# Optimization experiments

Measured on AMD Instinct MI355X. Metric: run time of the kernel, lower is better.

Reference implementation:

```python
import jax, jax.numpy as jnp
import numpy as np

B, D_IN, D_EXP, D_TOW, N_EXP, N_TASK = 16384, 1024, 1024, 512, 8, 4


def setup_inputs() -> dict:
    key = jax.random.key(0)
    ks = jax.random.split(key, 8)
    s_in = 1.0 / np.sqrt(D_IN)
    s_exp = 1.0 / np.sqrt(D_EXP)
    s_tow = 1.0 / np.sqrt(D_TOW)
    return {
        "x": jax.random.normal(ks[0], (B, D_IN), jnp.float32),
        # gate: ParameterList of num_experts vectors of size input_size -> [D_IN, N_EXP] matrix
        "gate_w": jax.random.normal(ks[1], (D_IN, N_EXP), jnp.float32) * s_in,
        # per-expert SLP: Linear(input_size, expert_size) + ReLU
        "exp_w": jax.random.normal(ks[2], (N_EXP, D_IN, D_EXP), jnp.float32) * s_in,
        "exp_b": jax.random.normal(ks[3], (N_EXP, D_EXP), jnp.float32) * 0.01,
        # per-task tower MLP: Linear(expert_size, tower_size) + ReLU + Linear(tower_size, 1)
        "tw1": jax.random.normal(ks[4], (N_TASK, D_EXP, D_TOW), jnp.float32) * s_exp,
        "tb1": jax.random.normal(ks[5], (N_TASK, D_TOW), jnp.float32) * 0.01,
        "tw2": jax.random.normal(ks[6], (N_TASK, D_TOW, 1), jnp.float32) * s_tow,
        "tb2": jax.random.normal(ks[7], (N_TASK, 1), jnp.float32) * 0.01,
    }


def reference(x, gate_w, exp_w, exp_b, tw1, tb1, tw2, tb2):
    # gates = x @ gate (no softmax in original)        [B, E]
    gates = x @ gate_w
    # all experts in one batched GEMM                  [E, B, D_exp]
    h = jax.nn.relu(jnp.einsum("bi,eid->ebd", x, exp_w) + exp_b[:, None, :])
    # fused gate-weighted combine (replaces the nested Python loops)
    shared = jnp.einsum("be,ebd->bd", gates, h)        # [B, D_exp]
    # per-task towers, batched over tasks
    t = jax.nn.relu(jnp.einsum("bd,tdh->tbh", shared, tw1) + tb1[:, None, :])
    outs = jnp.einsum("tbh,tho->tbo", t, tw2) + tb2[:, None, :]  # [T, B, 1]
    return outs
```

## Files before the change

### kernel.cpp

```cpp
#include <hip/hip_runtime.h>
#include <hip/hip_bf16.h>

#define B_DIM   16384
#define D_IN    1024
#define D_EXP   1024
#define D_TOW   512
#define N_EXPT  8
#define N_TASK  4

typedef _Float16 f16x8 __attribute__((ext_vector_type(8)));
typedef _Float16 f16x4 __attribute__((ext_vector_type(4)));
typedef float    f32x4 __attribute__((ext_vector_type(4)));

__device__ __forceinline__ void gll16(const void* g, void* l) {
  __builtin_amdgcn_global_load_lds(
      (const __attribute__((address_space(1))) unsigned int*)g,
      (__attribute__((address_space(3))) unsigned int*)l,
      16, 0, 0);
}

__device__ __forceinline__ f16x8 ldfrag(const _Float16* sM, int rowbase, int ks, int lane) {
  int rl = rowbase + (lane & 15);
  int ch = ((ks << 2) + (lane >> 4)) ^ (rl & 7);
  return *(const f16x8*)&sM[rl * 64 + ch * 8];
}

__global__ __launch_bounds__(256) void prep_x_kernel(
    const float* __restrict__ x, const float* __restrict__ gw,
    _Float16* __restrict__ xh, float* __restrict__ gates)
{
  __shared__ float sred[4][8];
  const int t = threadIdx.x;
  const long row = blockIdx.x;
  float4 v = ((const float4*)(x + row * D_IN))[t];
  f16x4 h;
  h[0] = (_Float16)v.x; h[1] = (_Float16)v.y; h[2] = (_Float16)v.z; h[3] = (_Float16)v.w;
  ((f16x4*)(xh + row * D_IN))[t] = h;

  float g[8];
#pragma unroll
  for (int e = 0; e < 8; ++e) g[e] = 0.f;
  const float* wp = gw + (size_t)t * 4 * 8;
  float xs[4] = {v.x, v.y, v.z, v.w};
#pragma unroll
  for (int j = 0; j < 4; ++j)
#pragma unroll
    for (int e = 0; e < 8; ++e) g[e] += xs[j] * wp[j * 8 + e];

#pragma unroll
  for (int e = 0; e < 8; ++e) {
    g[e] += __shfl_xor(g[e], 1);  g[e] += __shfl_xor(g[e], 2);
    g[e] += __shfl_xor(g[e], 4);  g[e] += __shfl_xor(g[e], 8);
    g[e] += __shfl_xor(g[e], 16); g[e] += __shfl_xor(g[e], 32);
  }
  if ((t & 63) == 0) {
#pragma unroll
    for (int e = 0; e < 8; ++e) sred[t >> 6][e] = g[e];
  }
  __syncthreads();
  if (t < 8) gates[row * 8 + t] = sred[0][t] + sred[1][t] + sred[2][t] + sred[3][t];
}

__global__ __launch_bounds__(256) void transpose_cvt_kernel(
    const float* __restrict__ in, _Float16* __restrict__ outp, int K, int N)
{
  __shared__ float tile[64][65];
  const int t = threadIdx.x;
  const int tx = t & 63, ty = t >> 6;
  const int n0 = blockIdx.x * 64;
  const int k0 = blockIdx.y * 64;
  const long s = blockIdx.z;
  const float* ip = in + s * (long)K * N;
  _Float16* op = outp + s * (long)K * N;
#pragma unroll
  for (int i = 0; i < 16; ++i) {
    int r = ty * 16 + i;
    tile[r][tx] = ip[(long)(k0 + r) * N + n0 + tx];
  }
  __syncthreads();
#pragma unroll
  for (int i = 0; i < 16; ++i) {
    int r = ty * 16 + i;
    op[(long)(n0 + r) * K + k0 + tx] = (_Float16)tile[tx][r];
  }
}

__global__ void init_out_kernel(float* __restrict__ out, const float* __restrict__ tb2) {
  int i = blockIdx.x * 256 + threadIdx.x;
  if (i < N_TASK * B_DIM) out[i] = tb2[i >> 14];
}

__global__ __launch_bounds__(256, 2) void moe_expert_kernel(
    const _Float16* __restrict__ xh,
    const _Float16* __restrict__ ewT,
    const float* __restrict__ expb,
    const float* __restrict__ gates,
    _Float16* __restrict__ shout)
{
  __shared__ alignas(16) _Float16 sA[128 * 64];
  __shared__ alignas(16) _Float16 sB[128 * 64];
  __shared__ float sG[128 * 8];
  const int t = threadIdx.x;
  const int lane = t & 63;
  const int wave = t >> 6;
  const int wm = wave >> 1, wn = wave & 1;
  const long row0 = (long)blockIdx.x * 128;
  const int col0 = blockIdx.y * 128;

#pragma unroll
  for (int i = 0; i < 4; ++i) sG[i * 256 + t] = gates[row0 * 8 + i * 256 + t];

  f32x4 shacc[4][4] = {};

  const char* gA0 = (const char*)(xh + row0 * D_IN);
  for (int e = 0; e < N_EXPT; ++e) {
    const char* gB0 = (const char*)(ewT + (size_t)e * D_IN * D_EXP + (size_t)col0 * D_IN);
    f32x4 acc[4][4] = {};
    for (int k0 = 0; k0 < D_IN; k0 += 64) {
#pragma unroll
      for (int r = 0; r < 4; ++r) {
        int b = r * 4096 + t * 16;
        int rowl = b >> 7;
        int sl = (b >> 4) & 7;
        int so = ((sl ^ (rowl & 7)) << 4);
        char* ldst = (char*)nullptr;
        ldst = (char*)sA + r * 4096 + ((t >> 6) << 10);
        gll16(gA0 + (size_t)k0 * 2 + (size_t)rowl * 2048 + so, ldst);
        ldst = (char*)sB + r * 4096 + ((t >> 6) << 10);
        gll16(gB0 + (size_t)k0 * 2 + (size_t)rowl * 2048 + so, ldst);
      }
      __syncthreads();
#pragma unroll
      for (int ks = 0; ks < 2; ++ks) {
        f16x8 af[4], bf[4];
#pragma unroll
        for (int m = 0; m < 4; ++m) af[m] = ldfrag(sA, wm * 64 + m * 16, ks, lane);
#pragma unroll
        for (int n = 0; n < 4; ++n) bf[n] = ldfrag(sB, wn * 64 + n * 16, ks, lane);
#pragma unroll
        for (int m = 0; m < 4; ++m)
#pragma unroll
          for (int n = 0; n < 4; ++n)
            acc[m][n] = __builtin_amdgcn_mfma_f32_16x16x32_f16(af[m], bf[n], acc[m][n], 0, 0, 0);
      }
      __syncthreads();
    }
#pragma unroll
    for (int n = 0; n < 4; ++n) {
      int col = col0 + wn * 64 + n * 16 + (lane & 15);
      float bias = expb[e * D_EXP + col];
#pragma unroll
      for (int m = 0; m < 4; ++m) {
        int rbase = wm * 64 + m * 16 + ((lane >> 4) << 2);
#pragma unroll
        for (int r = 0; r < 4; ++r) {
          float hv = acc[m][n][r] + bias;
          hv = hv > 0.f ? hv : 0.f;
          shacc[m][n][r] += sG[(rbase + r) * 8 + e] * hv;
        }
      }
    }
  }

#pragma unroll
  for (int m = 0; m < 4; ++m)
#pragma unroll
    for (int r = 0; r < 4; ++r) {
      long row = row0 + wm * 64 + m * 16 + ((lane >> 4) << 2) + r;
      _Float16* op = shout + row * D_EXP + col0 + wn * 64 + (lane & 15);
#pragma unroll
      for (int n = 0; n < 4; ++n) op[n * 16] = (_Float16)shacc[m][n][r];
    }
}

__global__ __launch_bounds__(256, 2) void moe_tower_kernel(
    const _Float16* __restrict__ sh,
    const _Float16* __restrict__ t1T,
    const float* __restrict__ tb1,
    const float* __restrict__ tw2,
    float* __restrict__ out)
{
  __shared__ alignas(16) _Float16 sA[128 * 64];
  __shared__ alignas(16) _Float16 sB[128 * 64];
  const int t = threadIdx.x;
  const int lane = t & 63;
  const int wave = t >> 6;
  const int wm = wave >> 1, wn = wave & 1;
  const long row0 = (long)blockIdx.x * 128;
  const int task = blockIdx.y >> 2;
  const int h0 = (blockIdx.y & 3) * 128;

  const char* gA0 = (const char*)(sh + row0 * D_EXP);
  const char* gB0 = (const char*)(t1T + (size_t)task * D_TOW * D_EXP + (size_t)h0 * D_EXP);

  f32x4 acc[4][4] = {};
  for (int k0 = 0; k0 < D_EXP; k0 += 64) {
#pragma unroll
    for (int r = 0; r < 4; ++r) {
      int b = r * 4096 + t * 16;
      int rowl = b >> 7;
      int sl = (b >> 4) & 7;
      int so = ((sl ^ (rowl & 7)) << 4);
      gll16(gA0 + (size_t)k0 * 2 + (size_t)rowl * 2048 + so,
            (char*)sA + r * 4096 + ((t >> 6) << 10));
      gll16(gB0 + (size_t)k0 * 2 + (size_t)rowl * 2048 + so,
            (char*)sB + r * 4096 + ((t >> 6) << 10));
    }
    __syncthreads();
#pragma unroll
    for (int ks = 0; ks < 2; ++ks) {
      f16x8 af[4], bf[4];
#pragma unroll
      for (int m = 0; m < 4; ++m) af[m] = ldfrag(sA, wm * 64 + m * 16, ks, lane);
#pragma unroll
      for (int n = 0; n < 4; ++n) bf[n] = ldfrag(sB, wn * 64 + n * 16, ks, lane);
#pragma unroll
      for (int m = 0; m < 4; ++m)
#pragma unroll
        for (int n = 0; n < 4; ++n)
          acc[m][n] = __builtin_amdgcn_mfma_f32_16x16x32_f16(af[m], bf[n], acc[m][n], 0, 0, 0);
    }
    __syncthreads();
  }

  float b1[4], w2[4];
#pragma unroll
  for (int n = 0; n < 4; ++n) {
    int col = h0 + wn * 64 + n * 16 + (lane & 15);
    b1[n] = tb1[task * D_TOW + col];
    w2[n] = tw2[task * D_TOW + col];
  }
#pragma unroll
  for (int m = 0; m < 4; ++m)
#pragma unroll
    for (int r = 0; r < 4; ++r) {
      float ssum = 0.f;
#pragma unroll
      for (int n = 0; n < 4; ++n) {
        float v = acc[m][n][r] + b1[n];
        v = v > 0.f ? v : 0.f;
        ssum += v * w2[n];
      }
      ssum += __shfl_xor(ssum, 1);
      ssum += __shfl_xor(ssum, 2);
      ssum += __shfl_xor(ssum, 4);
      ssum += __shfl_xor(ssum, 8);
      if ((lane & 15) == 0) {
        long row = row0 + wm * 64 + m * 16 + ((lane >> 4) << 2) + r;
        atomicAdd(&out[(size_t)task * B_DIM + row], ssum);
      }
    }
}

extern "C" void kernel_launch(void* const* d_in, const int* in_sizes, int n_in,
                              void* d_out, int out_size, void* d_ws, size_t ws_size,
                              hipStream_t stream) {
  const float* x    = (const float*)d_in[0];
  const float* gw   = (const float*)d_in[1];
  const float* expw = (const float*)d_in[2];
  const float* expb = (const float*)d_in[3];
  const float* tw1  = (const float*)d_in[4];
  const float* tb1  = (const float*)d_in[5];
  const float* tw2  = (const float*)d_in[6];
  const float* tb2  = (const float*)d_in[7];
  float* out = (float*)d_out;

  char* ws = (char*)d_ws;
  _Float16* xh  = (_Float16*)ws;  ws += (size_t)B_DIM * D_IN * 2;
  _Float16* ewT = (_Float16*)ws;  ws += (size_t)N_EXPT * D_IN * D_EXP * 2;
  _Float16* t1T = (_Float16*)ws;  ws += (size_t)N_TASK * D_TOW * D_EXP * 2;
  _Float16* shh = (_Float16*)ws;  ws += (size_t)B_DIM * D_EXP * 2;
  float* gates  = (float*)ws;     ws += (size_t)B_DIM * N_EXPT * 4;

  prep_x_kernel<<<B_DIM, 256, 0, stream>>>(x, gw, xh, gates);
  transpose_cvt_kernel<<<dim3(D_EXP / 64, D_IN / 64, N_EXPT), 256, 0, stream>>>(
      expw, ewT, D_IN, D_EXP);
  transpose_cvt_kernel<<<dim3(D_TOW / 64, D_EXP / 64, N_TASK), 256, 0, stream>>>(
      tw1, t1T, D_EXP, D_TOW);
  init_out_kernel<<<(N_TASK * B_DIM + 255) / 256, 256, 0, stream>>>(out, tb2);
  moe_expert_kernel<<<dim3(B_DIM / 128, D_EXP / 128), 256, 0, stream>>>(
      xh, ewT, expb, gates, shh);
  moe_tower_kernel<<<dim3(B_DIM / 128, (N_TASK * D_TOW) / 128), 256, 0, stream>>>(
      shh, t1T, tb1, tw2, out);
}
```

Before: 455.4 us.

## Triple-buffer LDS pipeline with 256-row tiles and 8 waves in MoE GEMMs

Both the expert and tower GEMM kernels now use 512-thread blocks covering 256 rows by 128 columns, so each B tile is shared across twice as many rows. Global-to-LDS loads go into a three-stage ring and are issued two steps ahead, with a single barrier and a partial vmcnt wait per step replacing the two syncthreads. The expert kernel flattens the expert and k loops into one pipelined loop, stages biases in LDS, and raises wave priority around the MFMA block. This costs about 147 KB of LDS per block, which limits how many blocks can sit on a CU.

Measured after the change: 493.5 us. 1.08x slower.

```diff
diff --git a/kernel.cpp b/kernel.cpp
--- a/kernel.cpp
+++ b/kernel.cpp
@@ -90,76 +90,108 @@
   if (i < N_TASK * B_DIM) out[i] = tb2[i >> 14];
 }
 
-__global__ __launch_bounds__(256, 2) void moe_expert_kernel(
+__global__ __launch_bounds__(512, 2) void moe_expert_kernel(
     const _Float16* __restrict__ xh,
     const _Float16* __restrict__ ewT,
     const float* __restrict__ expb,
     const float* __restrict__ gates,
     _Float16* __restrict__ shout)
 {
-  __shared__ alignas(16) _Float16 sA[128 * 64];
-  __shared__ alignas(16) _Float16 sB[128 * 64];
-  __shared__ float sG[128 * 8];
+  __shared__ alignas(16) _Float16 sAB[3][24576];
+  __shared__ float sG[256 * 8];
+  __shared__ float sBias[8 * 128];
   const int t = threadIdx.x;
   const int lane = t & 63;
   const int wave = t >> 6;
   const int wm = wave >> 1, wn = wave & 1;
-  const long row0 = (long)blockIdx.x * 128;
+  const long row0 = (long)blockIdx.x * 256;
   const int col0 = blockIdx.y * 128;
 
-#pragma unroll
-  for (int i = 0; i < 4; ++i) sG[i * 256 + t] = gates[row0 * 8 + i * 256 + t];
-
+  for (int i = t; i < 256 * 8; i += 512) sG[i] = gates[row0 * 8 + i];
+  for (int i = t; i < 8 * 128; i += 512)
+    sBias[i] = expb[(i >> 7) * D_EXP + col0 + (i & 127)];
+
+  const int so_t = (((t & 7) ^ ((t >> 3) & 7)) << 4);
+  const char* aBase = (const char*)xh + row0 * 2048 + (size_t)(t >> 3) * 2048 + so_t;
+  const char* bRoot = (const char*)ewT + (size_t)col0 * 2048 + (size_t)(t >> 3) * 2048 + so_t;
+
+  char* p0 = (char*)&sAB[0][0];
+  char* p1 = (char*)&sAB[1][0];
+  char* p2 = (char*)&sAB[2][0];
+
+  auto STAGE = [&](char* pS, int step) {
+    int e = step >> 4, kk = step & 15;
+    const char* ga = aBase + kk * 128;
+    const char* gb = bRoot + (size_t)e * (D_IN * D_EXP * 2) + kk * 128;
+#pragma unroll
+    for (int r = 0; r < 4; ++r)
+      gll16(ga + r * 131072, pS + r * 8192 + t * 16);
+#pragma unroll
+    for (int r = 0; r < 2; ++r)
+      gll16(gb + r * 131072, pS + 32768 + r * 8192 + t * 16);
+  };
+
+  __syncthreads();
+
+  char *pRead = p0, *pNext = p1, *pStage = p2;
+  STAGE(p0, 0);
+  STAGE(p1, 1);
+
+  f32x4 acc[4][4] = {};
   f32x4 shacc[4][4] = {};
 
-  const char* gA0 = (const char*)(xh + row0 * D_IN);
-  for (int e = 0; e < N_EXPT; ++e) {
-    const char* gB0 = (const char*)(ewT + (size_t)e * D_IN * D_EXP + (size_t)col0 * D_IN);
-    f32x4 acc[4][4] = {};
-    for (int k0 = 0; k0 < D_IN; k0 += 64) {
-#pragma unroll
-      for (int r = 0; r < 4; ++r) {
-        int b = r * 4096 + t * 16;
-        int rowl = b >> 7;
-        int sl = (b >> 4) & 7;
-        int so = ((sl ^ (rowl & 7)) << 4);
-        char* ldst = (char*)nullptr;
-        ldst = (char*)sA + r * 4096 + ((t >> 6) << 10);
-        gll16(gA0 + (size_t)k0 * 2 + (size_t)rowl * 2048 + so, ldst);
-        ldst = (char*)sB + r * 4096 + ((t >> 6) << 10);
-        gll16(gB0 + (size_t)k0 * 2 + (size_t)rowl * 2048 + so, ldst);
-      }
-      __syncthreads();
-#pragma unroll
-      for (int ks = 0; ks < 2; ++ks) {
-        f16x8 af[4], bf[4];
-#pragma unroll
-        for (int m = 0; m < 4; ++m) af[m] = ldfrag(sA, wm * 64 + m * 16, ks, lane);
-#pragma unroll
-        for (int n = 0; n < 4; ++n) bf[n] = ldfrag(sB, wn * 64 + n * 16, ks, lane);
-#pragma unroll
-        for (int m = 0; m < 4; ++m)
-#pragma unroll
-          for (int n = 0; n < 4; ++n)
-            acc[m][n] = __builtin_amdgcn_mfma_f32_16x16x32_f16(af[m], bf[n], acc[m][n], 0, 0, 0);
-      }
-      __syncthreads();
-    }
-#pragma unroll
-    for (int n = 0; n < 4; ++n) {
-      int col = col0 + wn * 64 + n * 16 + (lane & 15);
-      float bias = expb[e * D_EXP + col];
+  for (int i = 0; i < 128; ++i) {
+    if (i < 127) { asm volatile("s_waitcnt vmcnt(6)" ::: "memory"); }
+    else         { asm volatile("s_waitcnt vmcnt(0)" ::: "memory"); }
+    __builtin_amdgcn_s_barrier();
+    asm volatile("" ::: "memory");
+
+    if (i < 126) STAGE(pStage, i + 2);
+
+    const _Float16* bufA = (const _Float16*)pRead;
+    const _Float16* bufB = bufA + 16384;
+
+    __builtin_amdgcn_s_setprio(1);
+#pragma unroll
+    for (int ks = 0; ks < 2; ++ks) {
+      f16x8 af[4], bf[4];
+#pragma unroll
+      for (int m = 0; m < 4; ++m) af[m] = ldfrag(bufA, wm * 64 + m * 16, ks, lane);
+#pragma unroll
+      for (int n = 0; n < 4; ++n) bf[n] = ldfrag(bufB, wn * 64 + n * 16, ks, lane);
+#pragma unroll
+      for (int m = 0; m < 4; ++m)
+#pragma unroll
+        for (int n = 0; n < 4; ++n)
+          acc[m][n] = __builtin_amdgcn_mfma_f32_16x16x32_f16(af[m], bf[n], acc[m][n], 0, 0, 0);
+    }
+    __builtin_amdgcn_s_setprio(0);
+
+    if ((i & 15) == 15) {
+      const int e = i >> 4;
+      float gv[4][4];
 #pragma unroll
       for (int m = 0; m < 4; ++m) {
         int rbase = wm * 64 + m * 16 + ((lane >> 4) << 2);
 #pragma unroll
-        for (int r = 0; r < 4; ++r) {
-          float hv = acc[m][n][r] + bias;
-          hv = hv > 0.f ? hv : 0.f;
-          shacc[m][n][r] += sG[(rbase + r) * 8 + e] * hv;
-        }
+        for (int r = 0; r < 4; ++r) gv[m][r] = sG[(rbase + r) * 8 + e];
       }
-    }
+#pragma unroll
+      for (int n = 0; n < 4; ++n) {
+        float bias = sBias[e * 128 + wn * 64 + n * 16 + (lane & 15)];
+#pragma unroll
+        for (int m = 0; m < 4; ++m)
+#pragma unroll
+          for (int r = 0; r < 4; ++r) {
+            float hv = acc[m][n][r] + bias;
+            hv = hv > 0.f ? hv : 0.f;
+            shacc[m][n][r] += gv[m][r] * hv;
+            acc[m][n][r] = 0.f;
+          }
+      }
+    }
+
+    char* tmp = pRead; pRead = pNext; pNext = pStage; pStage = tmp;
   }
 
 #pragma unroll
@@ -173,54 +205,78 @@
     }
 }
 
-__global__ __launch_bounds__(256, 2) void moe_tower_kernel(
+__global__ __launch_bounds__(512, 2) void moe_tower_kernel(
     const _Float16* __restrict__ sh,
     const _Float16* __restrict__ t1T,
     const float* __restrict__ tb1,
     const float* __restrict__ tw2,
     float* __restrict__ out)
 {
-  __shared__ alignas(16) _Float16 sA[128 * 64];
-  __shared__ alignas(16) _Float16 sB[128 * 64];
+  __shared__ alignas(16) _Float16 sAB[3][24576];
   const int t = threadIdx.x;
   const int lane = t & 63;
   const int wave = t >> 6;
   const int wm = wave >> 1, wn = wave & 1;
-  const long row0 = (long)blockIdx.x * 128;
+  const long row0 = (long)blockIdx.x * 256;
   const int task = blockIdx.y >> 2;
   const int h0 = (blockIdx.y & 3) * 128;
 
-  const char* gA0 = (const char*)(sh + row0 * D_EXP);
-  const char* gB0 = (const char*)(t1T + (size_t)task * D_TOW * D_EXP + (size_t)h0 * D_EXP);
+  const int so_t = (((t & 7) ^ ((t >> 3) & 7)) << 4);
+  const char* aBase = (const char*)sh + row0 * 2048 + (size_t)(t >> 3) * 2048 + so_t;
+  const char* bBase = (const char*)t1T + (size_t)task * (D_TOW * D_EXP * 2)
+                      + (size_t)h0 * 2048 + (size_t)(t >> 3) * 2048 + so_t;
+
+  char* p0 = (char*)&sAB[0][0];
+  char* p1 = (char*)&sAB[1][0];
+  char* p2 = (char*)&sAB[2][0];
+
+  auto STAGE = [&](char* pS, int kk) {
+    const char* ga = aBase + kk * 128;
+    const char* gb = bBase + kk * 128;
+#pragma unroll
+    for (int r = 0; r < 4; ++r)
+      gll16(ga + r * 131072, pS + r * 8192 + t * 16);
+#pragma unroll
+    for (int r = 0; r < 2; ++r)
+      gll16(gb + r * 131072, pS + 32768 + r * 8192 + t * 16);
+  };
+
+  __syncthreads();
+
+  char *pRead = p0, *pNext = p1, *pStage = p2;
+  STAGE(p0, 0);
+  STAGE(p1, 1);
 
   f32x4 acc[4][4] = {};
-  for (int k0 = 0; k0 < D_EXP; k0 += 64) {
-#pragma unroll
-    for (int r = 0; r < 4; ++r) {
-      int b = r * 4096 + t * 16;
-      int rowl = b >> 7;
-      int sl = (b >> 4) & 7;
-      int so = ((sl ^ (rowl & 7)) << 4);
-      gll16(gA0 + (size_t)k0 * 2 + (size_t)rowl * 2048 + so,
-            (char*)sA + r * 4096 + ((t >> 6) << 10));
-      gll16(gB0 + (size_t)k0 * 2 + (size_t)rowl * 2048 + so,
-            (char*)sB + r * 4096 + ((t >> 6) << 10));
-    }
-    __syncthreads();
+
+  for (int i = 0; i < 16; ++i) {
+    if (i < 15) { asm volatile("s_waitcnt vmcnt(6)" ::: "memory"); }
+    else        { asm volatile("s_waitcnt vmcnt(0)" ::: "memory"); }
+    __builtin_amdgcn_s_barrier();
+    asm volatile("" ::: "memory");
+
+    if (i < 14) STAGE(pStage, i + 2);
+
+    const _Float16* bufA = (const _Float16*)pRead;
+    const _Float16* bufB = bufA + 16384;
+
+    __builtin_amdgcn_s_setprio(1);
 #pragma unroll
     for (int ks = 0; ks < 2; ++ks) {
       f16x8 af[4], bf[4];
 #pragma unroll
-      for (int m = 0; m < 4; ++m) af[m] = ldfrag(sA, wm * 64 + m * 16, ks, lane);
-#pragma unroll
-      for (int n = 0; n < 4; ++n) bf[n] = ldfrag(sB, wn * 64 + n * 16, ks, lane);
+      for (int m = 0; m < 4; ++m) af[m] = ldfrag(bufA, wm * 64 + m * 16, ks, lane);
+#pragma unroll
+      for (int n = 0; n < 4; ++n) bf[n] = ldfrag(bufB, wn * 64 + n * 16, ks, lane);
 #pragma unroll
       for (int m = 0; m < 4; ++m)
 #pragma unroll
         for (int n = 0; n < 4; ++n)
           acc[m][n] = __builtin_amdgcn_mfma_f32_16x16x32_f16(af[m], bf[n], acc[m][n], 0, 0, 0);
     }
-    __syncthreads();
+    __builtin_amdgcn_s_setprio(0);
+
+    char* tmp = pRead; pRead = pNext; pNext = pStage; pStage = tmp;
   }
 
   float b1[4], w2[4];
@@ -278,8 +334,8 @@
   transpose_cvt_kernel<<<dim3(D_TOW / 64, D_EXP / 64, N_TASK), 256, 0, stream>>>(
       tw1, t1T, D_EXP, D_TOW);
   init_out_kernel<<<(N_TASK * B_DIM + 255) / 256, 256, 0, stream>>>(out, tb2);
-  moe_expert_kernel<<<dim3(B_DIM / 128, D_EXP / 128), 256, 0, stream>>>(
+  moe_expert_kernel<<<dim3(B_DIM / 256, D_EXP / 128), 512, 0, stream>>>(
       xh, ewT, expb, gates, shh);
-  moe_tower_kernel<<<dim3(B_DIM / 128, (N_TASK * D_TOW) / 128), 256, 0, stream>>>(
+  moe_tower_kernel<<<dim3(B_DIM / 256, (N_TASK * D_TOW) / 128), 512, 0, stream>>>(
       shh, t1T, tb1, tw2, out);
 }
```
